# Performance work log

Measured on AMD Instinct MI355X. Metric: run time of the kernel, lower is better.

Reference implementation:

```python
import jax, jax.numpy as jnp
import numpy as np

D_MODEL = 1024
NUM_EXP = 64
EPS = 1e-9
B, L = 16, 2048


def setup_inputs() -> dict:
    key = jax.random.key(0)
    ks = jax.random.split(key, 12)
    s = 1.0 / np.sqrt(D_MODEL)
    inp = {
        "x": jax.random.normal(ks[0], (B, L, D_MODEL), dtype=jnp.float32),
        "n_indexes": jax.random.randint(ks[1], (B, NUM_EXP), 0, NUM_EXP),
        "mask": jax.random.randint(ks[2], (B, 1, L), 0, 2).astype(jnp.int32),
        "q_emb": jax.random.normal(ks[3], (NUM_EXP, D_MODEL), dtype=jnp.float32),
        "b_emb": jax.random.normal(ks[4], (NUM_EXP, D_MODEL), dtype=jnp.float32),
        "Wk": jax.random.normal(ks[5], (D_MODEL, D_MODEL), dtype=jnp.float32) * s,
        "bk": jnp.zeros((D_MODEL,), jnp.float32),
        "Wa": jax.random.normal(ks[6], (D_MODEL, D_MODEL), dtype=jnp.float32) * s,
        "ba": jnp.zeros((D_MODEL,), jnp.float32),
        "Wb": jax.random.normal(ks[7], (D_MODEL, D_MODEL), dtype=jnp.float32) * s,
        "bb": jnp.zeros((D_MODEL,), jnp.float32),
        "Ws": jax.random.normal(ks[8], (D_MODEL, D_MODEL), dtype=jnp.float32) * s,
        "bs": jnp.zeros((D_MODEL,), jnp.float32),
    }
    return inp


def reference(x, n_indexes, mask, q_emb, b_emb, Wk, bk, Wa, ba, Wb, bb, Ws, bs):
    # Dropout layers act as identity (eval mode).
    query_exp = q_emb[n_indexes]          # [B, E, D]
    bias_exp = b_emb[n_indexes]           # [B, E, D]
    x_key = x @ Wk.T + bk                 # [B, L, D]
    z = jnp.einsum('bed,bld->bel', query_exp, x_key) / np.sqrt(D_MODEL)  # [B, E, L]

    maskf = (mask != 0).astype(z.dtype)   # broadcast [B,1,L]
    class_a_fw = jax.nn.relu(z) * maskf
    class_b_fw = jax.nn.relu(-z) * maskf
    class_a_fw = class_a_fw / (class_a_fw.sum(-1, keepdims=True) + EPS)
    class_b_fw = class_b_fw / (class_b_fw.sum(-1, keepdims=True) + EPS)

    class_a = jnp.einsum('bel,bld->bed', class_a_fw, x @ Wa.T + ba) + bias_exp
    class_b = jnp.einsum('bel,bld->bed', class_b_fw, x @ Wb.T + bb) + bias_exp

    zt = jnp.swapaxes(z, -2, -1)          # [B, L, E]  (unmasked, as in source)
    class_a_bw = jax.nn.relu(zt)
    class_b_bw = jax.nn.relu(-zt)
    class_a_bw = class_a_bw / (class_a_bw.sum(-1, keepdims=True) + EPS)
    class_b_bw = class_b_bw / (class_b_bw.sum(-1, keepdims=True) + EPS)

    class_a = jnp.einsum('ble,bed->bld', class_a_bw, class_a)  # [B, L, D]
    class_b = jnp.einsum('ble,bed->bld', class_b_bw, class_b)

    selector = jax.nn.sigmoid(x @ Ws.T + bs)
    return selector * class_a + (1.0 - selector) * class_b
```

## Files before the change

kernel.cpp:

```cpp
#include <hip/hip_runtime.h>
#include <math.h>

#define D_MODEL 1024
#define NUM_EXP 64
#define B_SZ 16
#define L_SZ 2048

using bf16x8  = __attribute__((ext_vector_type(8))) __bf16;
using floatx4 = __attribute__((ext_vector_type(4))) float;
using ushort8 = __attribute__((ext_vector_type(8))) unsigned short;
using ushort4v = __attribute__((ext_vector_type(4))) unsigned short;

__device__ __forceinline__ unsigned short f2bf(float f) {
    union { float f; unsigned u; } x; x.f = f;
    unsigned r = (x.u + 0x7fffu + ((x.u >> 16) & 1u)) >> 16;
    return (unsigned short)r;
}
__device__ __forceinline__ float bf2f(unsigned short h) {
    union { unsigned u; float f; } x; x.u = ((unsigned)h) << 16;
    return x.f;
}

#define GLD16(gp, lp) __builtin_amdgcn_global_load_lds( \
    (const __attribute__((address_space(1))) unsigned int*)(gp), \
    (__attribute__((address_space(3))) unsigned int*)(lp), 16, 0, 0)

__global__ void k_convx(const float* __restrict__ in, unsigned short* __restrict__ outN,
                        unsigned short* __restrict__ outT)
{
    __shared__ unsigned short T[64][65];
    const int b = blockIdx.z;
    const int l0 = blockIdx.y * 64, c0 = blockIdx.x * 64;
    const int t = threadIdx.x;
    const int tr = t >> 4, tc = (t & 15) * 4;
    const float* src = in + ((long)b * L_SZ + l0) * D_MODEL + c0;
    unsigned short* dN = outN + ((long)b * L_SZ + l0) * D_MODEL + c0;
    #pragma unroll
    for (int i = 0; i < 4; i++) {
        int r = tr + i * 16;
        float4 v = *(const float4*)(src + (long)r * D_MODEL + tc);
        ushort4v u; u[0]=f2bf(v.x); u[1]=f2bf(v.y); u[2]=f2bf(v.z); u[3]=f2bf(v.w);
        *(ushort4v*)(dN + (long)r * D_MODEL + tc) = u;
        T[r][tc+0]=u[0]; T[r][tc+1]=u[1]; T[r][tc+2]=u[2]; T[r][tc+3]=u[3];
    }
    __syncthreads();
    unsigned short* dT = outT + ((long)b * D_MODEL + c0) * L_SZ + l0;
    #pragma unroll
    for (int i = 0; i < 4; i++) {
        int c = tr + i * 16;
        ushort4v u;
        u[0]=T[tc+0][c]; u[1]=T[tc+1][c]; u[2]=T[tc+2][c]; u[3]=T[tc+3][c];
        *(ushort4v*)(dT + (long)c * L_SZ + tc) = u;
    }
}

__global__ void k_transw(const float* __restrict__ in, unsigned short* __restrict__ outT)
{
    __shared__ unsigned short T[64][65];
    const int r0 = blockIdx.y * 64, c0 = blockIdx.x * 64;
    const int t = threadIdx.x;
    const int tr = t >> 4, tc = (t & 15) * 4;
    const float* src = in + (long)r0 * D_MODEL + c0;
    #pragma unroll
    for (int i = 0; i < 4; i++) {
        int r = tr + i * 16;
        float4 v = *(const float4*)(src + (long)r * D_MODEL + tc);
        T[r][tc+0]=f2bf(v.x); T[r][tc+1]=f2bf(v.y); T[r][tc+2]=f2bf(v.z); T[r][tc+3]=f2bf(v.w);
    }
    __syncthreads();
    unsigned short* dT = outT + ((long)c0) * D_MODEL + r0;
    #pragma unroll
    for (int i = 0; i < 4; i++) {
        int c = tr + i * 16;
        ushort4v u;
        u[0]=T[tc+0][c]; u[1]=T[tc+1][c]; u[2]=T[tc+2][c]; u[3]=T[tc+3][c];
        *(ushort4v*)(dT + (long)c * D_MODEL + tc) = u;
    }
}

__global__ void k_convert3(const float* __restrict__ a, const float* __restrict__ b,
                           const float* __restrict__ c,
                           unsigned short* __restrict__ oa, unsigned short* __restrict__ ob,
                           unsigned short* __restrict__ oc)
{
    long i = ((long)blockIdx.x * 256 + threadIdx.x) * 8;
    int which = (int)(i >> 20);
    long off = i & ((1L << 20) - 1);
    const float* src = which == 0 ? a : which == 1 ? b : c;
    unsigned short* dst = which == 0 ? oa : which == 1 ? ob : oc;
    float4 v0 = *(const float4*)(src + off);
    float4 v1 = *(const float4*)(src + off + 4);
    ushort8 r;
    r[0]=f2bf(v0.x); r[1]=f2bf(v0.y); r[2]=f2bf(v0.z); r[3]=f2bf(v0.w);
    r[4]=f2bf(v1.x); r[5]=f2bf(v1.y); r[6]=f2bf(v1.z); r[7]=f2bf(v1.w);
    *(ushort8*)(dst + off) = r;
}

__global__ void k_gather(const int* __restrict__ idx, const float* __restrict__ q_emb,
                         const float* __restrict__ b_emb, const float* __restrict__ bk,
                         unsigned short* __restrict__ qexp, float* __restrict__ bias_exp,
                         float* __restrict__ qbk)
{
    int be = blockIdx.x;
    int row = idx[be];
    int t = threadIdx.x;
    const float* qs = q_emb + (long)row * D_MODEL;
    const float* bsrc = b_emb + (long)row * D_MODEL;
    float4 q4 = *(const float4*)(qs + t * 4);
    float4 k4 = *(const float4*)(bk + t * 4);
    float4 b4 = *(const float4*)(bsrc + t * 4);
    ushort4v r; r[0]=f2bf(q4.x); r[1]=f2bf(q4.y); r[2]=f2bf(q4.z); r[3]=f2bf(q4.w);
    *(ushort4v*)(qexp + (long)be * D_MODEL + t * 4) = r;
    *(float4*)(bias_exp + (long)be * D_MODEL + t * 4) = b4;
    float p = q4.x*k4.x + q4.y*k4.y + q4.z*k4.z + q4.w*k4.w;
    #pragma unroll
    for (int o = 32; o > 0; o >>= 1) p += __shfl_down(p, o);
    __shared__ float red[4];
    if ((t & 63) == 0) red[t >> 6] = p;
    __syncthreads();
    if (t == 0) qbk[be] = red[0] + red[1] + red[2] + red[3];
}

__launch_bounds__(256)
__global__ void k_gemm_bt(const unsigned short* __restrict__ A,
                          const unsigned short* __restrict__ Bm,
                          const float* __restrict__ rowbias,
                          void* __restrict__ Cout,
                          int M, int N, int K, float scale, int flags,
                          long sA, long sB, long sC)
{
    __shared__ __align__(16) unsigned short As[64 * 32];
    __shared__ __align__(16) unsigned short Bs[64 * 32];
    const int bz = blockIdx.z;
    const unsigned short* Ab = A + (long)bz * sA;
    const unsigned short* Bb = Bm + (long)bz * sB;
    const int tid = threadIdx.x;
    const int wave = tid >> 6, lane = tid & 63;
    const int m0 = blockIdx.y * 64, n0 = blockIdx.x * 64;
    const int lrow = tid >> 2, lk = (tid & 3) * 8;
    const int q = lane >> 4, mr = lane & 15;

    floatx4 acc[4];
    floatx4 z4 = {0.f, 0.f, 0.f, 0.f};
    #pragma unroll
    for (int j = 0; j < 4; j++) acc[j] = z4;

    const unsigned short* Aptr = Ab + (long)(m0 + lrow) * K + lk;
    const unsigned short* Bptr = Bb + (long)(n0 + lrow) * K + lk;

    for (int k0 = 0; k0 < K; k0 += 32) {
        __syncthreads();
        *(ushort8*)&As[lrow * 32 + lk] = *(const ushort8*)(Aptr + k0);
        *(ushort8*)&Bs[lrow * 32 + lk] = *(const ushort8*)(Bptr + k0);
        __syncthreads();
        bf16x8 af = *(const bf16x8*)&As[(wave * 16 + mr) * 32 + q * 8];
        #pragma unroll
        for (int j = 0; j < 4; j++) {
            bf16x8 bfr = *(const bf16x8*)&Bs[(j * 16 + mr) * 32 + q * 8];
            acc[j] = __builtin_amdgcn_mfma_f32_16x16x32_bf16(af, bfr, acc[j], 0, 0, 0);
        }
    }
    #pragma unroll
    for (int j = 0; j < 4; j++) {
        int gn = n0 + j * 16 + mr;
        #pragma unroll
        for (int r = 0; r < 4; r++) {
            int gm = m0 + wave * 16 + q * 4 + r;
            float v = acc[j][r];
            if (rowbias) v += rowbias[(long)bz * M + gm];
            v *= scale;
            long cidx = (long)bz * sC + (long)gm * N + gn;
            if (flags & 1) ((unsigned short*)Cout)[cidx] = f2bf(v);
            else           ((float*)Cout)[cidx] = v;
        }
    }
}

__launch_bounds__(256)
__global__ void k_gemm_fw2(const unsigned short* __restrict__ A1,
                           const unsigned short* __restrict__ A2,
                           const unsigned short* __restrict__ Bt,
                           unsigned short* __restrict__ C1,
                           unsigned short* __restrict__ C2)
{
    __shared__ __align__(16) unsigned short As1[64 * 32];
    __shared__ __align__(16) unsigned short As2[64 * 32];
    __shared__ __align__(16) unsigned short Bs[64 * 32];
    const int bz = blockIdx.z;
    const int n0 = blockIdx.x * 64;
    const int tid = threadIdx.x;
    const int wave = tid >> 6, lane = tid & 63;
    const int lrow = tid >> 2, lk = (tid & 3) * 8;
    const int q = lane >> 4, mr = lane & 15;

    const unsigned short* a1p = A1 + ((long)bz * NUM_EXP + lrow) * L_SZ + lk;
    const unsigned short* a2p = A2 + ((long)bz * NUM_EXP + lrow) * L_SZ + lk;
    const unsigned short* bp  = Bt + ((long)bz * D_MODEL + n0 + lrow) * L_SZ + lk;

    floatx4 acc1[4], acc2[4];
    floatx4 z4 = {0.f, 0.f, 0.f, 0.f};
    #pragma unroll
    for (int j = 0; j < 4; j++) { acc1[j] = z4; acc2[j] = z4; }

    for (int k0 = 0; k0 < L_SZ; k0 += 32) {
        __syncthreads();
        *(ushort8*)&As1[lrow * 32 + lk] = *(const ushort8*)(a1p + k0);
        *(ushort8*)&As2[lrow * 32 + lk] = *(const ushort8*)(a2p + k0);
        *(ushort8*)&Bs[lrow * 32 + lk]  = *(const ushort8*)(bp + k0);
        __syncthreads();
        bf16x8 f1 = *(const bf16x8*)&As1[(wave * 16 + mr) * 32 + q * 8];
        bf16x8 f2 = *(const bf16x8*)&As2[(wave * 16 + mr) * 32 + q * 8];
        #pragma unroll
        for (int j = 0; j < 4; j++) {
            bf16x8 bb = *(const bf16x8*)&Bs[(j * 16 + mr) * 32 + q * 8];
            acc1[j] = __builtin_amdgcn_mfma_f32_16x16x32_bf16(f1, bb, acc1[j], 0, 0, 0);
            acc2[j] = __builtin_amdgcn_mfma_f32_16x16x32_bf16(f2, bb, acc2[j], 0, 0, 0);
        }
    }
    #pragma unroll
    for (int j = 0; j < 4; j++) {
        int gn = n0 + j * 16 + mr;
        #pragma unroll
        for (int r = 0; r < 4; r++) {
            int gm = wave * 16 + q * 4 + r;
            long cidx = ((long)bz * NUM_EXP + gm) * D_MODEL + gn;
            C1[cidx] = f2bf(acc1[j][r]);
            C2[cidx] = f2bf(acc2[j][r]);
        }
    }
}

__launch_bounds__(256)
__global__ void k_gemm_cls(const unsigned short* __restrict__ fwxA, const unsigned short* __restrict__ fwxB,
                           const unsigned short* __restrict__ Wa_, const unsigned short* __restrict__ Wb_,
                           const float* __restrict__ ba_, const float* __restrict__ bb_,
                           const float* __restrict__ wsA, const float* __restrict__ wsB,
                           const float* __restrict__ biasE,
                           unsigned short* __restrict__ aHi, unsigned short* __restrict__ aLo,
                           unsigned short* __restrict__ bHi, unsigned short* __restrict__ bLo)
{
    __shared__ __align__(16) unsigned short As[64 * 32];
    __shared__ __align__(16) unsigned short Bs[64 * 32];
    const int zz = blockIdx.z;
    const int side = zz >> 4, bz = zz & 15;
    const unsigned short* Ab = (side ? fwxB : fwxA) + (long)bz * NUM_EXP * D_MODEL;
    const unsigned short* Bb = side ? Wb_ : Wa_;
    const float* cb = side ? bb_ : ba_;
    const float* rw = (side ? wsB : wsA) + bz * NUM_EXP;
    const float* bE = biasE + (long)bz * NUM_EXP * D_MODEL;
    unsigned short* oHi = (side ? bHi : aHi) + (long)bz * NUM_EXP * D_MODEL;
    unsigned short* oLo = (side ? bLo : aLo) + (long)bz * NUM_EXP * D_MODEL;

    const int tid = threadIdx.x;
    const int wave = tid >> 6, lane = tid & 63;
    const int n0 = blockIdx.x * 64;
    const int lrow = tid >> 2, lk = (tid & 3) * 8;
    const int q = lane >> 4, mr = lane & 15;

    floatx4 acc[4];
    floatx4 z4 = {0.f, 0.f, 0.f, 0.f};
    #pragma unroll
    for (int j = 0; j < 4; j++) acc[j] = z4;

    const unsigned short* Aptr = Ab + (long)lrow * D_MODEL + lk;
    const unsigned short* Bptr = Bb + (long)(n0 + lrow) * D_MODEL + lk;

    for (int k0 = 0; k0 < D_MODEL; k0 += 32) {
        __syncthreads();
        *(ushort8*)&As[lrow * 32 + lk] = *(const ushort8*)(Aptr + k0);
        *(ushort8*)&Bs[lrow * 32 + lk] = *(const ushort8*)(Bptr + k0);
        __syncthreads();
        bf16x8 af = *(const bf16x8*)&As[(wave * 16 + mr) * 32 + q * 8];
        #pragma unroll
        for (int j = 0; j < 4; j++) {
            bf16x8 bfr = *(const bf16x8*)&Bs[(j * 16 + mr) * 32 + q * 8];
            acc[j] = __builtin_amdgcn_mfma_f32_16x16x32_bf16(af, bfr, acc[j], 0, 0, 0);
        }
    }
    #pragma unroll
    for (int j = 0; j < 4; j++) {
        int gn = n0 + j * 16 + mr;
        float cbv = cb[gn];
        #pragma unroll
        for (int r = 0; r < 4; r++) {
            int gm = wave * 16 + q * 4 + r;
            float v = acc[j][r] + rw[gm] * cbv + bE[(long)gm * D_MODEL + gn];
            unsigned short hi = f2bf(v);
            long tix = (long)gn * NUM_EXP + gm;
            oHi[tix] = hi;
            oLo[tix] = f2bf(v - bf2f(hi));
        }
    }
}

__launch_bounds__(512, 2)
__global__ void k_gemm_sel(const unsigned short* __restrict__ A,
                           const unsigned short* __restrict__ Bm,
                           const float* __restrict__ bias,
                           unsigned short* __restrict__ C)
{
    __shared__ __align__(16) unsigned short As[2][2][8192];
    __shared__ __align__(16) unsigned short Bs[2][2][8192];

    const int tid = threadIdx.x;
    const int wid = tid >> 6, lane = tid & 63;
    const int q = lane >> 4, mr = lane & 15;
    const int wm = wid >> 2, wn = wid & 3;
    const int kread = (q ^ ((mr >> 1) & 3)) * 8;

    const int bid = blockIdx.x;
    const int wg = (bid & 7) * 64 + (bid >> 3);
    const int m0 = (wg >> 2) * 256;
    const int n0 = (wg & 3) * 256;

    const unsigned short* Ag = A + (long)m0 * 1024;
    const unsigned short* Bg = Bm + (long)n0 * 1024;

    const int srow = tid >> 2;
    const int sgrp = (tid & 3) ^ ((srow >> 1) & 3);
    const long soff = (long)srow * 1024 + sgrp * 8;
    const int ldst = wid * 64 * 8;

    auto STAGE = [&](int g) {
        int tile = g >> 2; if (tile > 15) tile = 15;
        const int kh = (g >> 1) & 1, isB = g & 1;
        const unsigned short* src = (isB ? Bg : Ag) + (long)tile * 64 + kh * 32 + soff;
        unsigned short* dst = (isB ? &Bs[0][0][0] : &As[0][0][0])
                              + ((tile & 1) * 2 + kh) * 8192 + ldst;
        GLD16(src, dst);
        GLD16(src + 128 * 1024, dst + 4096);
    };

    floatx4 acc[8][4];
    floatx4 z4 = {0.f, 0.f, 0.f, 0.f};
    #pragma unroll
    for (int i = 0; i < 8; i++)
        #pragma unroll
        for (int j = 0; j < 4; j++) acc[i][j] = z4;

    STAGE(0); STAGE(1); STAGE(2); STAGE(3); STAGE(4); STAGE(5);
    asm volatile("s_waitcnt vmcnt(4)" ::: "memory");
    __builtin_amdgcn_s_barrier();

    for (int t = 0; t < 16; t++) {
        const unsigned short* Abuf = &As[t & 1][0][0];
        const unsigned short* Bbuf = &Bs[t & 1][0][0];
        bf16x8 bfr[4];
        #pragma unroll
        for (int p = 0; p < 4; p++) {
            const int kh = p >> 1, mh = p & 1;
            bf16x8 af[4];
            #pragma unroll
            for (int i = 0; i < 4; i++)
                af[i] = *(const bf16x8*)&Abuf[kh * 8192 +
                        (wm * 128 + mh * 64 + i * 16 + mr) * 32 + kread];
            if (mh == 0) {
                #pragma unroll
                for (int j = 0; j < 4; j++)
                    bfr[j] = *(const bf16x8*)&Bbuf[kh * 8192 +
                             (wn * 64 + j * 16 + mr) * 32 + kread];
            }
            STAGE(4 * t + p + 6);
            if (mh == 1) asm volatile("s_waitcnt vmcnt(8)" ::: "memory");
            __builtin_amdgcn_s_barrier();
            asm volatile("s_waitcnt lgkmcnt(0)" ::: "memory");
            __builtin_amdgcn_sched_barrier(0);
            __builtin_amdgcn_s_setprio(1);
            #pragma unroll
            for (int i = 0; i < 4; i++)
                #pragma unroll
                for (int j = 0; j < 4; j++)
                    acc[mh * 4 + i][j] = __builtin_amdgcn_mfma_f32_16x16x32_bf16(
                        af[i], bfr[j], acc[mh * 4 + i][j], 0, 0, 0);
            __builtin_amdgcn_s_setprio(0);
            __builtin_amdgcn_s_barrier();
            __builtin_amdgcn_sched_barrier(0);
        }
    }
    asm volatile("s_waitcnt vmcnt(0)" ::: "memory");

    #pragma unroll
    for (int i = 0; i < 8; i++) {
        #pragma unroll
        for (int j = 0; j < 4; j++) {
            const int gn = n0 + wn * 64 + j * 16 + mr;
            const float cbv = bias[gn];
            #pragma unroll
            for (int r = 0; r < 4; r++) {
                const int gm = m0 + wm * 128 + i * 16 + q * 4 + r;
                C[(long)gm * 1024 + gn] = f2bf(acc[i][j][r] + cbv);
            }
        }
    }
}

__global__ void k_fwnorm(const float* __restrict__ z, const int* __restrict__ mask,
                         unsigned short* __restrict__ a_fw, unsigned short* __restrict__ b_fw,
                         float* __restrict__ wsum_a, float* __restrict__ wsum_b)
{
    int be = blockIdx.x;
    int b = be >> 6;
    const float* zr = z + (long)be * L_SZ;
    const int* mr = mask + (long)b * L_SZ;
    int tid = threadIdx.x;
    float sa = 0.f, sb = 0.f;
    for (int l = tid; l < L_SZ; l += 256) {
        float v = zr[l];
        if (mr[l] != 0) { sa += fmaxf(v, 0.f); sb += fmaxf(-v, 0.f); }
    }
    #pragma unroll
    for (int o = 32; o > 0; o >>= 1) { sa += __shfl_down(sa, o); sb += __shfl_down(sb, o); }
    __shared__ float red[8];
    int wave = tid >> 6, lane = tid & 63;
    if (lane == 0) { red[wave] = sa; red[4 + wave] = sb; }
    __syncthreads();
    float ta = red[0] + red[1] + red[2] + red[3];
    float tb = red[4] + red[5] + red[6] + red[7];
    float ia = 1.f / (ta + 1e-9f), ib = 1.f / (tb + 1e-9f);
    if (tid == 0) { wsum_a[be] = ta * ia; wsum_b[be] = tb * ib; }
    for (int l = tid; l < L_SZ; l += 256) {
        float v = zr[l];
        float m = (mr[l] != 0) ? 1.f : 0.f;
        a_fw[(long)be * L_SZ + l] = f2bf(fmaxf(v, 0.f) * m * ia);
        b_fw[(long)be * L_SZ + l] = f2bf(fmaxf(-v, 0.f) * m * ib);
    }
}

__global__ void k_bwnorm(const float* __restrict__ z, unsigned short* __restrict__ a_bw,
                         unsigned short* __restrict__ b_bw)
{
    int r = blockIdx.x * 256 + threadIdx.x;
    int b = r >> 11, l = r & 2047;
    const float* zb = z + (long)b * NUM_EXP * L_SZ + l;
    float sa = 0.f, sb = 0.f;
    float va[NUM_EXP];
    #pragma unroll 8
    for (int e = 0; e < NUM_EXP; e++) {
        float v = zb[(long)e * L_SZ];
        va[e] = v;
        sa += fmaxf(v, 0.f); sb += fmaxf(-v, 0.f);
    }
    float ia = 1.f / (sa + 1e-9f), ib = 1.f / (sb + 1e-9f);
    unsigned short* ar = a_bw + (long)r * NUM_EXP;
    unsigned short* br = b_bw + (long)r * NUM_EXP;
    #pragma unroll 8
    for (int e = 0; e < NUM_EXP; e++) {
        float v = va[e];
        ar[e] = f2bf(fmaxf(v, 0.f) * ia);
        br[e] = f2bf(fmaxf(-v, 0.f) * ib);
    }
}

__launch_bounds__(256)
__global__ void k_final_mfma(const unsigned short* __restrict__ aw,
                             const unsigned short* __restrict__ bw,
                             const unsigned short* __restrict__ caHi,
                             const unsigned short* __restrict__ caLo,
                             const unsigned short* __restrict__ cbHi,
                             const unsigned short* __restrict__ cbLo,
                             const unsigned short* __restrict__ selbf,
                             float* __restrict__ out)
{
    __shared__ __align__(16) unsigned short Aa[64 * 72];
    __shared__ __align__(16) unsigned short Ab[64 * 72];
    __shared__ __align__(16) unsigned short BaH[64 * 72];
    __shared__ __align__(16) unsigned short BaL[64 * 72];
    __shared__ __align__(16) unsigned short BbH[64 * 72];
    __shared__ __align__(16) unsigned short BbL[64 * 72];
    const int bz = blockIdx.z;
    const int l0 = blockIdx.y * 64, d0 = blockIdx.x * 64;
    const int tid = threadIdx.x;
    const int wave = tid >> 6, lane = tid & 63;
    const int q = lane >> 4, mr = lane & 15;

    const unsigned short* awb = aw + ((long)bz * L_SZ + l0) * NUM_EXP;
    const unsigned short* bwb = bw + ((long)bz * L_SZ + l0) * NUM_EXP;
    const long cbase = ((long)bz * D_MODEL + d0) * NUM_EXP;

    #pragma unroll
    for (int c = 0; c < 2; c++) {
        int idx = c * 256 + tid;
        int row = idx >> 3, kc = (idx & 7) * 8;
        int lw = row * 72 + kc;
        long ga = (long)row * NUM_EXP + kc;
        *(ushort8*)&Aa[lw]  = *(const ushort8*)(awb + ga);
        *(ushort8*)&Ab[lw]  = *(const ushort8*)(bwb + ga);
        *(ushort8*)&BaH[lw] = *(const ushort8*)(caHi + cbase + ga);
        *(ushort8*)&BaL[lw] = *(const ushort8*)(caLo + cbase + ga);
        *(ushort8*)&BbH[lw] = *(const ushort8*)(cbHi + cbase + ga);
        *(ushort8*)&BbL[lw] = *(const ushort8*)(cbLo + cbase + ga);
    }
    __syncthreads();

    floatx4 accA[4], accB[4];
    floatx4 z4 = {0.f, 0.f, 0.f, 0.f};
    #pragma unroll
    for (int j = 0; j < 4; j++) { accA[j] = z4; accB[j] = z4; }

    #pragma unroll
    for (int ks = 0; ks < 2; ks++) {
        int ko = ks * 32 + q * 8;
        bf16x8 fa = *(const bf16x8*)&Aa[(wave * 16 + mr) * 72 + ko];
        bf16x8 fb = *(const bf16x8*)&Ab[(wave * 16 + mr) * 72 + ko];
        #pragma unroll
        for (int j = 0; j < 4; j++) {
            int bo = (j * 16 + mr) * 72 + ko;
            accA[j] = __builtin_amdgcn_mfma_f32_16x16x32_bf16(fa, *(const bf16x8*)&BaH[bo], accA[j], 0, 0, 0);
            accA[j] = __builtin_amdgcn_mfma_f32_16x16x32_bf16(fa, *(const bf16x8*)&BaL[bo], accA[j], 0, 0, 0);
            accB[j] = __builtin_amdgcn_mfma_f32_16x16x32_bf16(fb, *(const bf16x8*)&BbH[bo], accB[j], 0, 0, 0);
            accB[j] = __builtin_amdgcn_mfma_f32_16x16x32_bf16(fb, *(const bf16x8*)&BbL[bo], accB[j], 0, 0, 0);
        }
    }

    #pragma unroll
    for (int j = 0; j < 4; j++) {
        #pragma unroll
        for (int r = 0; r < 4; r++) {
            int gl = l0 + wave * 16 + q * 4 + r;
            int gd = d0 + j * 16 + mr;
            long o = ((long)bz * L_SZ + gl) * D_MODEL + gd;
            float s = 1.f / (1.f + __expf(-bf2f(selbf[o])));
            out[o] = s * accA[j][r] + (1.f - s) * accB[j][r];
        }
    }
}

extern "C" void kernel_launch(void* const* d_in, const int* in_sizes, int n_in,
                              void* d_out, int out_size, void* d_ws, size_t ws_size,
                              hipStream_t stream)
{
    const float* x     = (const float*)d_in[0];
    const int*   nidx  = (const int*)d_in[1];
    const int*   mask  = (const int*)d_in[2];
    const float* q_emb = (const float*)d_in[3];
    const float* b_emb = (const float*)d_in[4];
    const float* Wk    = (const float*)d_in[5];
    const float* bk    = (const float*)d_in[6];
    const float* Wa    = (const float*)d_in[7];
    const float* ba    = (const float*)d_in[8];
    const float* Wb    = (const float*)d_in[9];
    const float* bb    = (const float*)d_in[10];
    const float* Ws    = (const float*)d_in[11];
    const float* bs    = (const float*)d_in[12];
    float* out = (float*)d_out;

    constexpr long BLD = (long)B_SZ * L_SZ * D_MODEL;
    constexpr long BEL = (long)B_SZ * NUM_EXP * L_SZ;
    constexpr long BED = (long)B_SZ * NUM_EXP * D_MODEL;
    constexpr long DD  = (long)D_MODEL * D_MODEL;

    char* w = (char*)d_ws;
    size_t off = 0;
    auto carve = [&](size_t bytes) { char* p = w + off; off += (bytes + 255) & ~(size_t)255; return p; };
    unsigned short* x_bf   = (unsigned short*)carve(BLD * 2);
    unsigned short* x_bfT  = (unsigned short*)carve(BLD * 2);
    unsigned short* wkT_bf = (unsigned short*)carve(DD * 2);
    unsigned short* wa_bf  = (unsigned short*)carve(DD * 2);
    unsigned short* wb_bf  = (unsigned short*)carve(DD * 2);
    unsigned short* ws_bf  = (unsigned short*)carve(DD * 2);
    unsigned short* qexp   = (unsigned short*)carve(BED * 2);
    float*          bias_e = (float*)carve(BED * 4);
    float*          qbk    = (float*)carve(B_SZ * NUM_EXP * 4);
    unsigned short* qk     = (unsigned short*)carve(BED * 2);
    float*          z      = (float*)carve(BEL * 4);
    unsigned short* a_fw   = (unsigned short*)carve(BEL * 2);
    unsigned short* b_fw   = (unsigned short*)carve(BEL * 2);
    float*          wsum_a = (float*)carve(B_SZ * NUM_EXP * 4);
    float*          wsum_b = (float*)carve(B_SZ * NUM_EXP * 4);
    unsigned short* a_bw   = (unsigned short*)carve(BEL * 2);
    unsigned short* b_bw   = (unsigned short*)carve(BEL * 2);
    unsigned short* fwx_a  = (unsigned short*)carve(BED * 2);
    unsigned short* fwx_b  = (unsigned short*)carve(BED * 2);
    unsigned short* caHi   = (unsigned short*)carve(BED * 2);
    unsigned short* caLo   = (unsigned short*)carve(BED * 2);
    unsigned short* cbHi   = (unsigned short*)carve(BED * 2);
    unsigned short* cbLo   = (unsigned short*)carve(BED * 2);
    if (ws_size < off) return;
    unsigned short* selbf = x_bfT;

    k_convx<<<dim3(16, 32, B_SZ), 256, 0, stream>>>(x, x_bf, x_bfT);
    k_transw<<<dim3(16, 16), 256, 0, stream>>>(Wk, wkT_bf);
    k_convert3<<<(3 * DD) / 2048, 256, 0, stream>>>(Wa, Wb, Ws, wa_bf, wb_bf, ws_bf);
    k_gather<<<B_SZ * NUM_EXP, 256, 0, stream>>>(nidx, q_emb, b_emb, bk, qexp, bias_e, qbk);

    k_gemm_bt<<<dim3(16, 1, B_SZ), 256, 0, stream>>>(qexp, wkT_bf, nullptr, qk,
        NUM_EXP, D_MODEL, D_MODEL, 1.f, 1, (long)NUM_EXP * D_MODEL, 0, (long)NUM_EXP * D_MODEL);

    k_gemm_bt<<<dim3(32, 1, B_SZ), 256, 0, stream>>>(qk, x_bf, qbk, z,
        NUM_EXP, L_SZ, D_MODEL, 1.f / 32.f, 0,
        (long)NUM_EXP * D_MODEL, (long)L_SZ * D_MODEL, (long)NUM_EXP * L_SZ);

    k_fwnorm<<<B_SZ * NUM_EXP, 256, 0, stream>>>(z, mask, a_fw, b_fw, wsum_a, wsum_b);
    k_bwnorm<<<(B_SZ * L_SZ) / 256, 256, 0, stream>>>(z, a_bw, b_bw);

    k_gemm_fw2<<<dim3(16, 1, B_SZ), 256, 0, stream>>>(a_fw, b_fw, x_bfT, fwx_a, fwx_b);

    k_gemm_sel<<<512, 512, 0, stream>>>(x_bf, ws_bf, bs, selbf);

    k_gemm_cls<<<dim3(16, 1, 32), 256, 0, stream>>>(fwx_a, fwx_b, wa_bf, wb_bf, ba, bb,
        wsum_a, wsum_b, bias_e, caHi, caLo, cbHi, cbLo);

    k_final_mfma<<<dim3(16, 32, B_SZ), 256, 0, stream>>>(a_bw, b_bw, caHi, caLo, cbHi, cbLo, selbf, out);
}
```

Baseline: 548.4 us.

## Split-K fw2 GEMM across two thread groups and restructure sel GEMM pipeline

The fw2 GEMM now runs 512 threads per block, with two 256-thread groups each covering half of the L reduction. The partial sums are combined through shared memory before the bf16 store, which doubles wave-level parallelism for a grid of only 256 blocks. The selector GEMM main loop is reorganised into one iteration per K tile, with prefetches issued per half-tile, finer lgkmcnt waits and fewer barriers, so LDS reads overlap more with MFMA. The costs are extra shared memory for the reduction buffer and more fragile hand-tuned waitcnt ordering.

```diff
diff --git a/kernel.cpp b/kernel.cpp
--- a/kernel.cpp
+++ b/kernel.cpp
@@ -176,56 +176,74 @@
     }
 }
 
-__launch_bounds__(256)
+__launch_bounds__(512)
 __global__ void k_gemm_fw2(const unsigned short* __restrict__ A1,
                            const unsigned short* __restrict__ A2,
                            const unsigned short* __restrict__ Bt,
                            unsigned short* __restrict__ C1,
                            unsigned short* __restrict__ C2)
 {
-    __shared__ __align__(16) unsigned short As1[64 * 32];
-    __shared__ __align__(16) unsigned short As2[64 * 32];
-    __shared__ __align__(16) unsigned short Bs[64 * 32];
+    __shared__ __align__(16) unsigned short As1[2][64 * 32];
+    __shared__ __align__(16) unsigned short As2[2][64 * 32];
+    __shared__ __align__(16) unsigned short Bs[2][64 * 32];
+    __shared__ float Red[2][64][65];
     const int bz = blockIdx.z;
     const int n0 = blockIdx.x * 64;
     const int tid = threadIdx.x;
-    const int wave = tid >> 6, lane = tid & 63;
-    const int lrow = tid >> 2, lk = (tid & 3) * 8;
+    const int grp = tid >> 8;
+    const int gtid = tid & 255;
+    const int wave = gtid >> 6, lane = tid & 63;
+    const int lrow = gtid >> 2, lk = (gtid & 3) * 8;
     const int q = lane >> 4, mr = lane & 15;
-
-    const unsigned short* a1p = A1 + ((long)bz * NUM_EXP + lrow) * L_SZ + lk;
-    const unsigned short* a2p = A2 + ((long)bz * NUM_EXP + lrow) * L_SZ + lk;
-    const unsigned short* bp  = Bt + ((long)bz * D_MODEL + n0 + lrow) * L_SZ + lk;
+    const int kb = grp * (L_SZ / 2);
+
+    const unsigned short* a1p = A1 + ((long)bz * NUM_EXP + lrow) * L_SZ + kb + lk;
+    const unsigned short* a2p = A2 + ((long)bz * NUM_EXP + lrow) * L_SZ + kb + lk;
+    const unsigned short* bp  = Bt + ((long)bz * D_MODEL + n0 + lrow) * L_SZ + kb + lk;
 
     floatx4 acc1[4], acc2[4];
     floatx4 z4 = {0.f, 0.f, 0.f, 0.f};
     #pragma unroll
     for (int j = 0; j < 4; j++) { acc1[j] = z4; acc2[j] = z4; }
 
-    for (int k0 = 0; k0 < L_SZ; k0 += 32) {
+    for (int k0 = 0; k0 < L_SZ / 2; k0 += 32) {
         __syncthreads();
-        *(ushort8*)&As1[lrow * 32 + lk] = *(const ushort8*)(a1p + k0);
-        *(ushort8*)&As2[lrow * 32 + lk] = *(const ushort8*)(a2p + k0);
-        *(ushort8*)&Bs[lrow * 32 + lk]  = *(const ushort8*)(bp + k0);
+        *(ushort8*)&As1[grp][lrow * 32 + lk] = *(const ushort8*)(a1p + k0);
+        *(ushort8*)&As2[grp][lrow * 32 + lk] = *(const ushort8*)(a2p + k0);
+        *(ushort8*)&Bs[grp][lrow * 32 + lk]  = *(const ushort8*)(bp + k0);
         __syncthreads();
-        bf16x8 f1 = *(const bf16x8*)&As1[(wave * 16 + mr) * 32 + q * 8];
-        bf16x8 f2 = *(const bf16x8*)&As2[(wave * 16 + mr) * 32 + q * 8];
+        bf16x8 f1 = *(const bf16x8*)&As1[grp][(wave * 16 + mr) * 32 + q * 8];
+        bf16x8 f2 = *(const bf16x8*)&As2[grp][(wave * 16 + mr) * 32 + q * 8];
         #pragma unroll
         for (int j = 0; j < 4; j++) {
-            bf16x8 bb = *(const bf16x8*)&Bs[(j * 16 + mr) * 32 + q * 8];
+            bf16x8 bb = *(const bf16x8*)&Bs[grp][(j * 16 + mr) * 32 + q * 8];
             acc1[j] = __builtin_amdgcn_mfma_f32_16x16x32_bf16(f1, bb, acc1[j], 0, 0, 0);
             acc2[j] = __builtin_amdgcn_mfma_f32_16x16x32_bf16(f2, bb, acc2[j], 0, 0, 0);
         }
     }
-    #pragma unroll
-    for (int j = 0; j < 4; j++) {
-        int gn = n0 + j * 16 + mr;
-        #pragma unroll
-        for (int r = 0; r < 4; r++) {
-            int gm = wave * 16 + q * 4 + r;
-            long cidx = ((long)bz * NUM_EXP + gm) * D_MODEL + gn;
-            C1[cidx] = f2bf(acc1[j][r]);
-            C2[cidx] = f2bf(acc2[j][r]);
+    __syncthreads();
+    if (grp == 1) {
+        #pragma unroll
+        for (int j = 0; j < 4; j++)
+            #pragma unroll
+            for (int r = 0; r < 4; r++) {
+                int gm = wave * 16 + q * 4 + r;
+                Red[0][gm][j * 16 + mr] = acc1[j][r];
+                Red[1][gm][j * 16 + mr] = acc2[j][r];
+            }
+    }
+    __syncthreads();
+    if (grp == 0) {
+        #pragma unroll
+        for (int j = 0; j < 4; j++) {
+            int gn = n0 + j * 16 + mr;
+            #pragma unroll
+            for (int r = 0; r < 4; r++) {
+                int gm = wave * 16 + q * 4 + r;
+                long cidx = ((long)bz * NUM_EXP + gm) * D_MODEL + gn;
+                C1[cidx] = f2bf(acc1[j][r] + Red[0][gm][j * 16 + mr]);
+                C2[cidx] = f2bf(acc2[j][r] + Red[1][gm][j * 16 + mr]);
+            }
         }
     }
 }
@@ -321,9 +339,8 @@
     const long soff = (long)srow * 1024 + sgrp * 8;
     const int ldst = wid * 64 * 8;
 
-    auto STAGE = [&](int g) {
-        int tile = g >> 2; if (tile > 15) tile = 15;
-        const int kh = (g >> 1) & 1, isB = g & 1;
+    auto STAGE_H = [&](int tile, int kh, int isB) {
+        if (tile > 15) tile = 15;
         const unsigned short* src = (isB ? Bg : Ag) + (long)tile * 64 + kh * 32 + soff;
         unsigned short* dst = (isB ? &Bs[0][0][0] : &As[0][0][0])
                               + ((tile & 1) * 2 + kh) * 8192 + ldst;
@@ -338,44 +355,75 @@
         #pragma unroll
         for (int j = 0; j < 4; j++) acc[i][j] = z4;
 
-    STAGE(0); STAGE(1); STAGE(2); STAGE(3); STAGE(4); STAGE(5);
+    STAGE_H(0, 0, 0); STAGE_H(0, 0, 1);
+    STAGE_H(0, 1, 0); STAGE_H(0, 1, 1);
+    STAGE_H(1, 0, 0); STAGE_H(1, 0, 1);
     asm volatile("s_waitcnt vmcnt(4)" ::: "memory");
     __builtin_amdgcn_s_barrier();
 
     for (int t = 0; t < 16; t++) {
-        const unsigned short* Abuf = &As[t & 1][0][0];
-        const unsigned short* Bbuf = &Bs[t & 1][0][0];
-        bf16x8 bfr[4];
-        #pragma unroll
-        for (int p = 0; p < 4; p++) {
-            const int kh = p >> 1, mh = p & 1;
-            bf16x8 af[4];
+        const unsigned short* Ab_ = &As[t & 1][0][0];
+        const unsigned short* Bb_ = &Bs[t & 1][0][0];
+        bf16x8 b0[4], b1[4], a0[4], a1[4];
+        #pragma unroll
+        for (int j = 0; j < 4; j++)
+            b0[j] = *(const bf16x8*)&Bb_[(wn * 64 + j * 16 + mr) * 32 + kread];
+        #pragma unroll
+        for (int i = 0; i < 4; i++)
+            a0[i] = *(const bf16x8*)&Ab_[(wm * 128 + i * 16 + mr) * 32 + kread];
+        STAGE_H(t + 1, 1, 0); STAGE_H(t + 1, 1, 1);
+        #pragma unroll
+        for (int j = 0; j < 4; j++)
+            b1[j] = *(const bf16x8*)&Bb_[8192 + (wn * 64 + j * 16 + mr) * 32 + kread];
+        asm volatile("s_waitcnt lgkmcnt(4)" ::: "memory");
+        __builtin_amdgcn_sched_barrier(0);
+        __builtin_amdgcn_s_setprio(1);
+        #pragma unroll
+        for (int i = 0; i < 4; i++)
             #pragma unroll
-            for (int i = 0; i < 4; i++)
-                af[i] = *(const bf16x8*)&Abuf[kh * 8192 +
-                        (wm * 128 + mh * 64 + i * 16 + mr) * 32 + kread];
-            if (mh == 0) {
-                #pragma unroll
-                for (int j = 0; j < 4; j++)
-                    bfr[j] = *(const bf16x8*)&Bbuf[kh * 8192 +
-                             (wn * 64 + j * 16 + mr) * 32 + kread];
-            }
-            STAGE(4 * t + p + 6);
-            if (mh == 1) asm volatile("s_waitcnt vmcnt(8)" ::: "memory");
-            __builtin_amdgcn_s_barrier();
-            asm volatile("s_waitcnt lgkmcnt(0)" ::: "memory");
-            __builtin_amdgcn_sched_barrier(0);
-            __builtin_amdgcn_s_setprio(1);
+            for (int j = 0; j < 4; j++)
+                acc[i][j] = __builtin_amdgcn_mfma_f32_16x16x32_bf16(a0[i], b0[j], acc[i][j], 0, 0, 0);
+        __builtin_amdgcn_s_setprio(0);
+        #pragma unroll
+        for (int i = 0; i < 4; i++)
+            a1[i] = *(const bf16x8*)&Ab_[(wm * 128 + 64 + i * 16 + mr) * 32 + kread];
+        asm volatile("s_waitcnt lgkmcnt(0)" ::: "memory");
+        __builtin_amdgcn_sched_barrier(0);
+        __builtin_amdgcn_s_setprio(1);
+        #pragma unroll
+        for (int i = 0; i < 4; i++)
             #pragma unroll
-            for (int i = 0; i < 4; i++)
-                #pragma unroll
-                for (int j = 0; j < 4; j++)
-                    acc[mh * 4 + i][j] = __builtin_amdgcn_mfma_f32_16x16x32_bf16(
-                        af[i], bfr[j], acc[mh * 4 + i][j], 0, 0, 0);
-            __builtin_amdgcn_s_setprio(0);
-            __builtin_amdgcn_s_barrier();
-            __builtin_amdgcn_sched_barrier(0);
-        }
+            for (int j = 0; j < 4; j++)
+                acc[4 + i][j] = __builtin_amdgcn_mfma_f32_16x16x32_bf16(a1[i], b0[j], acc[4 + i][j], 0, 0, 0);
+        __builtin_amdgcn_s_setprio(0);
+        __builtin_amdgcn_s_barrier();
+        STAGE_H(t + 2, 0, 0); STAGE_H(t + 2, 0, 1);
+        #pragma unroll
+        for (int i = 0; i < 4; i++)
+            a0[i] = *(const bf16x8*)&Ab_[8192 + (wm * 128 + i * 16 + mr) * 32 + kread];
+        #pragma unroll
+        for (int i = 0; i < 4; i++)
+            a1[i] = *(const bf16x8*)&Ab_[8192 + (wm * 128 + 64 + i * 16 + mr) * 32 + kread];
+        asm volatile("s_waitcnt vmcnt(4)" ::: "memory");
+        asm volatile("s_waitcnt lgkmcnt(4)" ::: "memory");
+        __builtin_amdgcn_sched_barrier(0);
+        __builtin_amdgcn_s_setprio(1);
+        #pragma unroll
+        for (int i = 0; i < 4; i++)
+            #pragma unroll
+            for (int j = 0; j < 4; j++)
+                acc[i][j] = __builtin_amdgcn_mfma_f32_16x16x32_bf16(a0[i], b1[j], acc[i][j], 0, 0, 0);
+        __builtin_amdgcn_s_setprio(0);
+        asm volatile("s_waitcnt lgkmcnt(0)" ::: "memory");
+        __builtin_amdgcn_sched_barrier(0);
+        __builtin_amdgcn_s_setprio(1);
+        #pragma unroll
+        for (int i = 0; i < 4; i++)
+            #pragma unroll
+            for (int j = 0; j < 4; j++)
+                acc[4 + i][j] = __builtin_amdgcn_mfma_f32_16x16x32_bf16(a1[i], b1[j], acc[4 + i][j], 0, 0, 0);
+        __builtin_amdgcn_s_setprio(0);
+        __builtin_amdgcn_s_barrier();
     }
     asm volatile("s_waitcnt vmcnt(0)" ::: "memory");
 
@@ -593,7 +641,7 @@
     k_fwnorm<<<B_SZ * NUM_EXP, 256, 0, stream>>>(z, mask, a_fw, b_fw, wsum_a, wsum_b);
     k_bwnorm<<<(B_SZ * L_SZ) / 256, 256, 0, stream>>>(z, a_bw, b_bw);
 
-    k_gemm_fw2<<<dim3(16, 1, B_SZ), 256, 0, stream>>>(a_fw, b_fw, x_bfT, fwx_a, fwx_b);
+    k_gemm_fw2<<<dim3(16, 1, B_SZ), 512, 0, stream>>>(a_fw, b_fw, x_bfT, fwx_a, fwx_b);
 
     k_gemm_sel<<<512, 512, 0, stream>>>(x_bf, ws_bf, bs, selbf);
 
```

Result: no change. 546.2 us (-0.4%).
